# Kernel optimization log

Measured on AMD Instinct MI355X. Metric: run time of the kernel, lower is better.

## Reference

```python
import math
import jax, jax.numpy as jnp
import numpy as np

B, T, D, S = 4, 8192, 1024, 32  # batch, seq, dim, num_slots; segment L = T // S


def setup_inputs() -> dict:
    key = jax.random.key(0)
    ks = jax.random.split(key, 11)
    d_inv_sqrt = D ** -0.5
    return {
        "x": jax.random.normal(ks[0], (B, T, D), jnp.float32),
        "gate_w": jax.random.normal(ks[1], (D, D), jnp.float32) * d_inv_sqrt,
        "gate_b": jnp.zeros((D,), jnp.float32),
        "read_q_w": jax.random.normal(ks[2], (D, D), jnp.float32) * 0.02,
        "read_k_w": jax.random.normal(ks[3], (D, D), jnp.float32) * 0.02,
        "read_v_w": jax.random.normal(ks[4], (D, D), jnp.float32) * 0.02,
        "output_w": jax.random.normal(ks[5], (D, D), jnp.float32) * d_inv_sqrt,
        "memory_slots": jax.random.normal(ks[6], (S, D), jnp.float32) * 0.02,
        "write_q_w": jax.random.normal(ks[7], (D, D), jnp.float32) * 0.02,
        "write_k_w": jax.random.normal(ks[8], (D, D), jnp.float32) * 0.02,
        "write_v_w": jax.random.normal(ks[9], (D, D), jnp.float32) * 0.02,
    }


def reference(x, gate_w, gate_b, read_q_w, read_k_w, read_v_w, output_w,
              memory_slots, write_q_w, write_k_w, write_v_w):
    b, t, d = x.shape
    s = memory_slots.shape[0]
    L = t // s  # segment length
    scale = 1.0 / math.sqrt(d)

    h = x @ gate_w.T + gate_b  # [B,T,D] gate pre-activation

    # --- write: per-slot attention over that slot's segment (block-diagonal) ---
    q = memory_slots @ write_q_w.T                      # [S,D]
    xs = x.reshape(b, s, L, d)                          # [B,S,L,D]
    k = xs @ write_k_w.T                                # [B,S,L,D]
    v = xs @ write_v_w.T                                # [B,S,L,D]
    wqk = jnp.einsum('sd,bsld->bsl', q, k) * scale      # [B,S,L]
    wattn = jax.nn.softmax(wqk, axis=-1)
    memory = jnp.einsum('bsl,bsld->bsd', wattn, v)      # [B,S,D]

    # --- read: masked cross-attention from tokens to memory slots ---
    rq = x @ read_q_w.T                                 # [B,T,D]
    rk = memory @ read_k_w.T                            # [B,S,D]
    rv = memory @ read_v_w.T                            # [B,S,D]
    rqk = jnp.einsum('btd,bsd->bts', rq, rk) * scale    # [B,T,S]
    seg = jnp.arange(t) // L                            # token -> segment index
    mask = seg[:, None] <= jnp.arange(s)[None, :]       # [T,S]; attend to slots >= own segment
    rqk = jnp.where(mask[None, :, :], rqk, -jnp.inf)
    rattn = jax.nn.softmax(rqk, axis=-1)
    read = jnp.einsum('bts,bsd->btd', rattn, rv)        # [B,T,D]

    y = x + jax.nn.sigmoid(h) * read
    out = y @ output_w.T
    return out, memory
```

## Files before the change

kernel.cpp:

```cpp
#include <hip/hip_runtime.h>
#include <stdint.h>

#define TB 4
#define TT 8192
#define TD 1024
#define TS 32
#define TL 256
#define BT 32768

typedef unsigned short u16;
typedef __bf16 bf16x8 __attribute__((ext_vector_type(8)));
typedef float f32x4 __attribute__((ext_vector_type(4)));

typedef uint32_t u32_g __attribute__((address_space(1)));
typedef uint32_t u32_l __attribute__((address_space(3)));

#define VMWAIT(N) asm volatile("s_waitcnt vmcnt(" #N ")" ::: "memory")
#define LGKM0()   asm volatile("s_waitcnt lgkmcnt(0)" ::: "memory")

__device__ __forceinline__ u16 f2b(float f){
  union { float f; uint32_t u; } a; a.f = f;
  uint32_t r = a.u + 0x7FFFu + ((a.u >> 16) & 1u);
  return (u16)(r >> 16);
}
__device__ __forceinline__ float b2f(u16 u){
  union { uint32_t u; float f; } a; a.u = ((uint32_t)u) << 16;
  return a.f;
}
__device__ __forceinline__ void gll16(const void* g, void* l){
  __builtin_amdgcn_global_load_lds((const u32_g*)g, (u32_l*)l, 16, 0, 0);
}

__global__ void k_tran(const float* __restrict__ w0, const float* __restrict__ w1,
                       const float* __restrict__ w2, const float* __restrict__ w3,
                       const float* __restrict__ w4, const float* __restrict__ ms,
                       u16* __restrict__ t0, u16* __restrict__ t1,
                       u16* __restrict__ t2, u16* __restrict__ t3,
                       u16* __restrict__ t4, u16* __restrict__ msb){
  int tid = threadIdx.x, z = blockIdx.z;
  if (z == 5){
    int i = (blockIdx.y*16 + blockIdx.x)*256 + tid;
    if (i < 8192){
      float4 v = ((const float4*)ms)[i];
      ushort4 u; u.x=f2b(v.x); u.y=f2b(v.y); u.z=f2b(v.z); u.w=f2b(v.w);
      ((ushort4*)msb)[i] = u;
    }
    return;
  }
  const float* src = (z==0)?w0:(z==1)?w1:(z==2)?w2:(z==3)?w3:w4;
  u16* dst = (z==0)?t0:(z==1)?t1:(z==2)?t2:(z==3)?t3:t4;
  __shared__ float sT[64][65];
  int r0 = blockIdx.y*64, c0 = blockIdx.x*64;
  int lr = tid >> 2, lc = (tid & 3)*16;
  #pragma unroll
  for (int j=0; j<4; ++j){
    float4 v = *(const float4*)(src + (size_t)(r0+lr)*TD + c0 + lc + j*4);
    sT[lr][lc+j*4+0]=v.x; sT[lr][lc+j*4+1]=v.y; sT[lr][lc+j*4+2]=v.z; sT[lr][lc+j*4+3]=v.w;
  }
  __syncthreads();
  int oc = tid >> 2, orh = (tid & 3)*16;
  #pragma unroll
  for (int j=0; j<4; ++j){
    ushort4 u;
    u.x = f2b(sT[orh+j*4+0][oc]);
    u.y = f2b(sT[orh+j*4+1][oc]);
    u.z = f2b(sT[orh+j*4+2][oc]);
    u.w = f2b(sT[orh+j*4+3][oc]);
    *(ushort4*)(dst + (size_t)(c0+oc)*TD + r0 + orh + j*4) = u;
  }
}

__global__ __launch_bounds__(512) void k_smmw(
    const u16* __restrict__ A0, const u16* __restrict__ W0, u16* __restrict__ O0, int tr0, float s0,
    const u16* __restrict__ A1, const u16* __restrict__ W1, u16* __restrict__ O1, int tr1, float s1){
  const u16 *A, *W; u16* O; int tr; float sc;
  if (blockIdx.z == 0){ A=A0; W=W0; O=O0; tr=tr0; sc=s0; }
  else                { A=A1; W=W1; O=O1; tr=tr1; sc=s1; }
  int tid = threadIdx.x, lane = tid & 63, wv = tid >> 6;
  int r15 = lane & 15, kg = lane >> 4;
  int wr = wv >> 2, wc = wv & 3;
  int m0 = blockIdx.y*128 + wr*64;
  int n0 = blockIdx.x*128 + wc*32;
  const u16* ap = A + (size_t)(m0 + r15)*TD + kg*8;
  const u16* bp = W + (size_t)(n0 + r15)*TD + kg*8;
  f32x4 acc[4][2];
  #pragma unroll
  for (int i=0;i<4;i++){ f32x4 z={0,0,0,0}; acc[i][0]=z; acc[i][1]=z; }
  #pragma unroll 2
  for (int k0=0; k0<TD; k0+=32){
    bf16x8 b0 = *(const bf16x8*)(bp + k0);
    bf16x8 b1 = *(const bf16x8*)(bp + 16*TD + k0);
    bf16x8 a0 = *(const bf16x8*)(ap + k0);
    bf16x8 a1 = *(const bf16x8*)(ap + 16*TD + k0);
    bf16x8 a2 = *(const bf16x8*)(ap + 32*TD + k0);
    bf16x8 a3 = *(const bf16x8*)(ap + 48*TD + k0);
    acc[0][0] = __builtin_amdgcn_mfma_f32_16x16x32_bf16(a0, b0, acc[0][0], 0,0,0);
    acc[0][1] = __builtin_amdgcn_mfma_f32_16x16x32_bf16(a0, b1, acc[0][1], 0,0,0);
    acc[1][0] = __builtin_amdgcn_mfma_f32_16x16x32_bf16(a1, b0, acc[1][0], 0,0,0);
    acc[1][1] = __builtin_amdgcn_mfma_f32_16x16x32_bf16(a1, b1, acc[1][1], 0,0,0);
    acc[2][0] = __builtin_amdgcn_mfma_f32_16x16x32_bf16(a2, b0, acc[2][0], 0,0,0);
    acc[2][1] = __builtin_amdgcn_mfma_f32_16x16x32_bf16(a2, b1, acc[2][1], 0,0,0);
    acc[3][0] = __builtin_amdgcn_mfma_f32_16x16x32_bf16(a3, b0, acc[3][0], 0,0,0);
    acc[3][1] = __builtin_amdgcn_mfma_f32_16x16x32_bf16(a3, b1, acc[3][1], 0,0,0);
  }
  #pragma unroll
  for (int mf=0; mf<4; ++mf){
    #pragma unroll
    for (int nf=0; nf<2; ++nf){
      int n = n0 + nf*16 + r15;
      #pragma unroll
      for (int qq=0; qq<4; ++qq){
        float v = acc[mf][nf][qq]*sc;
        int m = m0 + mf*16 + kg*4 + qq;
        if (tr) O[(size_t)n*TD + m] = f2b(v);
        else    O[(size_t)m*TD + n] = f2b(v);
      }
    }
  }
}

__global__ __launch_bounds__(512) void k_qk32(const u16* __restrict__ msb, const u16* __restrict__ WzT,
                                              float* __restrict__ qkp){
  int tid = threadIdx.x, lane = tid & 63, wv = tid >> 6;
  int r15 = lane & 15, kg = lane >> 4;
  int n0 = blockIdx.x*128 + wv*16;
  int kbase = blockIdx.y*512;
  const u16* ap = msb + (size_t)r15*TD + kbase + kg*8;
  const u16* bp = WzT + (size_t)(n0 + r15)*TD + kbase + kg*8;
  f32x4 a0 = {0,0,0,0}, a1 = {0,0,0,0};
  #pragma unroll 4
  for (int k0=0; k0<512; k0+=32){
    bf16x8 b  = *(const bf16x8*)(bp + k0);
    bf16x8 x0 = *(const bf16x8*)(ap + k0);
    bf16x8 x1 = *(const bf16x8*)(ap + 16*TD + k0);
    a0 = __builtin_amdgcn_mfma_f32_16x16x32_bf16(x0, b, a0, 0,0,0);
    a1 = __builtin_amdgcn_mfma_f32_16x16x32_bf16(x1, b, a1, 0,0,0);
  }
  const float sc = 1.0f/32.0f;
  float* o = qkp + (size_t)blockIdx.y*32768;
  #pragma unroll
  for (int qq=0; qq<4; ++qq){
    o[(size_t)(kg*4 + qq)*TD + n0 + r15]      = a0[qq]*sc;
    o[(size_t)(16 + kg*4 + qq)*TD + n0 + r15] = a1[qq]*sc;
  }
}

__global__ void k_convdot(const float* __restrict__ x, const float* __restrict__ qkp,
                          u16* __restrict__ xb, float* __restrict__ wqk,
                          const float* __restrict__ s0, const float* __restrict__ s1,
                          const float* __restrict__ s2, const float* __restrict__ s3,
                          const float* __restrict__ s4,
                          u16* __restrict__ d0, u16* __restrict__ d1,
                          u16* __restrict__ d2, u16* __restrict__ d3,
                          u16* __restrict__ d4){
  int tid = threadIdx.x;
  if (blockIdx.x >= 2048){
    int i = (blockIdx.x - 2048)*256 + tid;
    int mi = i >> 18, j = i & 262143;
    const float* src; u16* dst;
    if      (mi == 0){ src = s0; dst = d0; }
    else if (mi == 1){ src = s1; dst = d1; }
    else if (mi == 2){ src = s2; dst = d2; }
    else if (mi == 3){ src = s3; dst = d3; }
    else             { src = s4; dst = d4; }
    float4 v = ((const float4*)src)[j];
    ushort4 u; u.x=f2b(v.x); u.y=f2b(v.y); u.z=f2b(v.z); u.w=f2b(v.w);
    ((ushort4*)dst)[j] = u;
    return;
  }
  int lane = tid & 63, wv = tid >> 6;
  long bt0 = (long)blockIdx.x * 16;
  int sseg = (int)((bt0 & (TT-1)) >> 8);
  float qv[16];
  #pragma unroll
  for (int i=0;i<4;i++){
    const float* qp = qkp + (size_t)sseg*TD + i*256 + lane*4;
    float4 ta = *(const float4*)qp;
    float4 tb = *(const float4*)(qp + 32768);
    qv[i*4+0]=ta.x+tb.x; qv[i*4+1]=ta.y+tb.y; qv[i*4+2]=ta.z+tb.z; qv[i*4+3]=ta.w+tb.w;
  }
  for (int tok = wv; tok < 16; tok += 4){
    long bt = bt0 + tok;
    const float* xr = x + bt*TD;
    float dot = 0.f;
    #pragma unroll
    for (int i=0;i<4;i++){
      float4 t = *(const float4*)(xr + i*256 + lane*4);
      ushort4 u; u.x=f2b(t.x); u.y=f2b(t.y); u.z=f2b(t.z); u.w=f2b(t.w);
      *(ushort4*)(xb + bt*TD + i*256 + lane*4) = u;
      dot += t.x*qv[i*4] + t.y*qv[i*4+1] + t.z*qv[i*4+2] + t.w*qv[i*4+3];
    }
    #pragma unroll
    for (int o=32;o;o>>=1) dot += __shfl_xor(dot, o);
    if (lane == 0) wqk[bt] = dot;
  }
}

__global__ __launch_bounds__(512) void k_wattn_smm(
    const float* __restrict__ wqk, const u16* __restrict__ xb, u16* __restrict__ xbarb,
    const u16* __restrict__ A1, const u16* __restrict__ W1, u16* __restrict__ O1,
    const u16* __restrict__ A2, const u16* __restrict__ W2, u16* __restrict__ O2){
  __shared__ float sw[2][TL];
  __shared__ float red[2][8];
  __shared__ f32x4 part[2][4][64];
  int tid = threadIdx.x;
  if (blockIdx.x < 256){
    int u = tid >> 8;
    int unit = blockIdx.x*2 + u;
    int bs = unit >> 2, dch = unit & 3;
    int b = bs >> 5, s = bs & 31;
    int t2 = tid & 255, lane = t2 & 63, wv = t2 >> 6;
    long base = (long)b*TT + (long)s*TL;
    float v = wqk[base + t2];
    float m = v;
    #pragma unroll
    for (int o=32;o;o>>=1) m = fmaxf(m, __shfl_xor(m, o));
    if (lane == 0) red[u][wv] = m;
    __syncthreads();
    m = fmaxf(fmaxf(red[u][0], red[u][1]), fmaxf(red[u][2], red[u][3]));
    float e = __expf(v - m);
    float sm = e;
    #pragma unroll
    for (int o=32;o;o>>=1) sm += __shfl_xor(sm, o);
    if (lane == 0) red[u][4+wv] = sm;
    __syncthreads();
    sm = red[u][4]+red[u][5]+red[u][6]+red[u][7];
    sw[u][t2] = e / sm;
    __syncthreads();
    int d = dch*256 + lane*4;
    const u16* xp = xb + (base + wv*64)*TD + d;
    f32x4 acc = {0,0,0,0};
    #pragma unroll 8
    for (int i=0; i<64; ++i){
      float w = sw[u][wv*64 + i];
      ushort4 uu = *(const ushort4*)(xp + (size_t)i*TD);
      acc[0] += w*b2f(uu.x); acc[1] += w*b2f(uu.y); acc[2] += w*b2f(uu.z); acc[3] += w*b2f(uu.w);
    }
    part[u][wv][lane] = acc;
    __syncthreads();
    if (wv == 0){
      f32x4 t0 = part[u][0][lane], t1 = part[u][1][lane], t2v = part[u][2][lane], t3 = part[u][3][lane];
      ushort4 o;
      o.x = f2b(t0[0]+t1[0]+t2v[0]+t3[0]);
      o.y = f2b(t0[1]+t1[1]+t2v[1]+t3[1]);
      o.z = f2b(t0[2]+t1[2]+t2v[2]+t3[2]);
      o.w = f2b(t0[3]+t1[3]+t2v[3]+t3[3]);
      *(ushort4*)(xbarb + ((size_t)b*TS + s)*TD + d) = o;
    }
    return;
  }
  int bi = blockIdx.x - 256;
  const u16 *A, *W; u16* O; int tr;
  if (bi < 64){ A=A1; W=W1; O=O1; tr=0; }
  else        { A=A2; W=W2; O=O2; tr=1; bi -= 64; }
  int by = bi >> 3, bx = bi & 7;
  int lane = tid & 63, wv = tid >> 6;
  int r15 = lane & 15, kg = lane >> 4;
  int wr = wv >> 2, wc = wv & 3;
  int m0 = by*128 + wr*64;
  int n0 = bx*128 + wc*32;
  const u16* ap = A + (size_t)(m0 + r15)*TD + kg*8;
  const u16* bp = W + (size_t)(n0 + r15)*TD + kg*8;
  f32x4 acc[4][2];
  #pragma unroll
  for (int i=0;i<4;i++){ f32x4 z={0,0,0,0}; acc[i][0]=z; acc[i][1]=z; }
  #pragma unroll 2
  for (int k0=0; k0<TD; k0+=32){
    bf16x8 b0 = *(const bf16x8*)(bp + k0);
    bf16x8 b1 = *(const bf16x8*)(bp + 16*TD + k0);
    bf16x8 a0 = *(const bf16x8*)(ap + k0);
    bf16x8 a1 = *(const bf16x8*)(ap + 16*TD + k0);
    bf16x8 a2 = *(const bf16x8*)(ap + 32*TD + k0);
    bf16x8 a3 = *(const bf16x8*)(ap + 48*TD + k0);
    acc[0][0] = __builtin_amdgcn_mfma_f32_16x16x32_bf16(a0, b0, acc[0][0], 0,0,0);
    acc[0][1] = __builtin_amdgcn_mfma_f32_16x16x32_bf16(a0, b1, acc[0][1], 0,0,0);
    acc[1][0] = __builtin_amdgcn_mfma_f32_16x16x32_bf16(a1, b0, acc[1][0], 0,0,0);
    acc[1][1] = __builtin_amdgcn_mfma_f32_16x16x32_bf16(a1, b1, acc[1][1], 0,0,0);
    acc[2][0] = __builtin_amdgcn_mfma_f32_16x16x32_bf16(a2, b0, acc[2][0], 0,0,0);
    acc[2][1] = __builtin_amdgcn_mfma_f32_16x16x32_bf16(a2, b1, acc[2][1], 0,0,0);
    acc[3][0] = __builtin_amdgcn_mfma_f32_16x16x32_bf16(a3, b0, acc[3][0], 0,0,0);
    acc[3][1] = __builtin_amdgcn_mfma_f32_16x16x32_bf16(a3, b1, acc[3][1], 0,0,0);
  }
  #pragma unroll
  for (int mf=0; mf<4; ++mf){
    #pragma unroll
    for (int nf=0; nf<2; ++nf){
      int n = n0 + nf*16 + r15;
      #pragma unroll
      for (int qq=0; qq<4; ++qq){
        float v = acc[mf][nf][qq];
        int m = m0 + mf*16 + kg*4 + qq;
        if (tr) O[(size_t)n*TD + m] = f2b(v);
        else    O[(size_t)m*TD + n] = f2b(v);
      }
    }
  }
}

__global__ __launch_bounds__(512) void k_xbar3(const u16* __restrict__ xbarb,
                                               const u16* __restrict__ Wv, const u16* __restrict__ WdT,
                                               const u16* __restrict__ We,
                                               float* __restrict__ memo, u16* __restrict__ rkb,
                                               u16* __restrict__ rvT){
  int z = blockIdx.z;
  const u16* W = (z==0) ? Wv : (z==1) ? WdT : We;
  int tid = threadIdx.x, lane = tid & 63, wv = tid >> 6;
  int r15 = lane & 15, kg = lane >> 4;
  int wr = wv >> 2, wc = wv & 3;
  int n0 = blockIdx.x*128 + wc*32;
  const u16* ap = xbarb + (size_t)(wr*64 + r15)*TD + kg*8;
  const u16* bp = W + (size_t)(n0 + r15)*TD + kg*8;
  f32x4 acc[4][2];
  #pragma unroll
  for (int i=0;i<4;i++){ f32x4 zz={0,0,0,0}; acc[i][0]=zz; acc[i][1]=zz; }
  #pragma unroll 2
  for (int k0=0; k0<TD; k0+=32){
    bf16x8 b0 = *(const bf16x8*)(bp + k0);
    bf16x8 b1 = *(const bf16x8*)(bp + 16*TD + k0);
    bf16x8 a0 = *(const bf16x8*)(ap + k0);
    bf16x8 a1 = *(const bf16x8*)(ap + 16*TD + k0);
    bf16x8 a2 = *(const bf16x8*)(ap + 32*TD + k0);
    bf16x8 a3 = *(const bf16x8*)(ap + 48*TD + k0);
    acc[0][0] = __builtin_amdgcn_mfma_f32_16x16x32_bf16(a0, b0, acc[0][0], 0,0,0);
    acc[0][1] = __builtin_amdgcn_mfma_f32_16x16x32_bf16(a0, b1, acc[0][1], 0,0,0);
    acc[1][0] = __builtin_amdgcn_mfma_f32_16x16x32_bf16(a1, b0, acc[1][0], 0,0,0);
    acc[1][1] = __builtin_amdgcn_mfma_f32_16x16x32_bf16(a1, b1, acc[1][1], 0,0,0);
    acc[2][0] = __builtin_amdgcn_mfma_f32_16x16x32_bf16(a2, b0, acc[2][0], 0,0,0);
    acc[2][1] = __builtin_amdgcn_mfma_f32_16x16x32_bf16(a2, b1, acc[2][1], 0,0,0);
    acc[3][0] = __builtin_amdgcn_mfma_f32_16x16x32_bf16(a3, b0, acc[3][0], 0,0,0);
    acc[3][1] = __builtin_amdgcn_mfma_f32_16x16x32_bf16(a3, b1, acc[3][1], 0,0,0);
  }
  #pragma unroll
  for (int mf=0; mf<4; ++mf){
    #pragma unroll
    for (int nf=0; nf<2; ++nf){
      int n = n0 + nf*16 + r15;
      #pragma unroll
      for (int qq=0; qq<4; ++qq){
        float v = acc[mf][nf][qq];
        int m = wr*64 + mf*16 + kg*4 + qq;
        if (z == 0)      memo[(size_t)m*TD + n] = v;
        else if (z == 1) rkb[(size_t)m*TD + n] = f2b(v);
        else             rvT[((size_t)(m>>5)*TD + n)*TS + (m&31)] = f2b(v);
      }
    }
  }
}

template<bool SIG>
__global__ __launch_bounds__(512, 2) void k_gemm(const u16* __restrict__ A, const u16* __restrict__ Bw,
                                                 const float* __restrict__ bias, void* __restrict__ Cp,
                                                 const u16* __restrict__ rkb, const u16* __restrict__ rvT){
  __shared__ __align__(16) char sL[131072];
  int tid = threadIdx.x, lane = tid & 63, wv = tid >> 6;
  int bid = blockIdx.x;
  int wg = ((bid & 7) << 6) | (bid >> 3);
  int nt = wg & 3, mt = wg >> 2;
  int m0 = mt*256, n0 = nt*256;
  int wr = wv >> 2, wc = wv & 3;
  int r15 = lane & 15, kg = lane >> 4;
  int smin = (m0 & (TT-1)) >> 8;
  bool wcP = SIG && ((wr == 0) ? (wc < 2) : (wc >= 2));

  int ard[8], brd[4];
  #pragma unroll
  for (int i=0;i<8;i++){ int row = wr*128 + i*16 + r15; ard[i] = row*128 + ((kg ^ (row&7))<<4); }
  #pragma unroll
  for (int j=0;j<4;j++){ int row = wc*64  + j*16 + r15; brd[j] = row*128 + ((kg ^ (row&7))<<4); }

  const u16* asrc[4]; const u16* bsrc[4]; int ldst[4];
  #pragma unroll
  for (int r=0;r<4;r++){
    int Sp  = r*512 + tid;
    int row = Sp >> 3;
    int kq  = (Sp & 7) ^ (row & 7);
    asrc[r] = A  + (size_t)(m0 + row)*TD + kq*8;
    bsrc[r] = Bw + (size_t)(n0 + row)*TD + kq*8;
    ldst[r] = Sp*16;
  }
  const u16* rkp = rkb + (size_t)((m0 >> 13)*TS + (wc&1)*16 + r15)*TD + kg*8;

  f32x4 acc[8][4];
  #pragma unroll
  for (int i=0;i<8;i++){
    #pragma unroll
    for (int j=0;j<4;j++){ f32x4 z = {0,0,0,0}; acc[i][j] = z; }
  }
  f32x4 pacc[8];
  if constexpr (SIG){
    #pragma unroll
    for (int i=0;i<8;i++){ f32x4 z = {0,0,0,0}; pacc[i] = z; }
  }

  auto stage = [&](int t){
    char* slot = sL + (size_t)(t&1)*65536;
    int k0 = t*64;
    #pragma unroll
    for (int r=0;r<4;r++) gll16(asrc[r] + k0, slot + ldst[r]);
    #pragma unroll
    for (int r=0;r<4;r++) gll16(bsrc[r] + k0, slot + 32768 + ldst[r]);
  };

  auto compute = [&](int t, bf16x8 rk0, bf16x8 rk1){
    const char* sa = sL + (size_t)(t&1)*65536;
    const char* sb = sa + 32768;
    bf16x8 bfg[4], af[4];
    #pragma unroll
    for (int j=0;j<4;j++) bfg[j] = *(const bf16x8*)(sb + brd[j]);
    #pragma unroll
    for (int i=0;i<4;i++) af[i] = *(const bf16x8*)(sa + ard[i]);
    LGKM0();
    __builtin_amdgcn_sched_barrier(0);
    __builtin_amdgcn_s_setprio(1);
    #pragma unroll
    for (int i=0;i<4;i++){
      #pragma unroll
      for (int j=0;j<4;j++)
        acc[i][j] = __builtin_amdgcn_mfma_f32_16x16x32_bf16(af[i], bfg[j], acc[i][j], 0,0,0);
    }
    if constexpr (SIG){
      if (wcP){
        #pragma unroll
        for (int i=0;i<4;i++) pacc[i] = __builtin_amdgcn_mfma_f32_16x16x32_bf16(af[i], rk0, pacc[i], 0,0,0);
      }
    }
    __builtin_amdgcn_s_setprio(0);
    bf16x8 af2[4];
    #pragma unroll
    for (int i=0;i<4;i++) af2[i] = *(const bf16x8*)(sa + (ard[4+i]));
    LGKM0();
    __builtin_amdgcn_sched_barrier(0);
    __builtin_amdgcn_s_setprio(1);
    #pragma unroll
    for (int i=0;i<4;i++){
      #pragma unroll
      for (int j=0;j<4;j++)
        acc[4+i][j] = __builtin_amdgcn_mfma_f32_16x16x32_bf16(af2[i], bfg[j], acc[4+i][j], 0,0,0);
    }
    if constexpr (SIG){
      if (wcP){
        #pragma unroll
        for (int i=0;i<4;i++) pacc[4+i] = __builtin_amdgcn_mfma_f32_16x16x32_bf16(af2[i], rk0, pacc[4+i], 0,0,0);
      }
    }
    __builtin_amdgcn_s_setprio(0);
    bf16x8 bfh[4], ag[4];
    #pragma unroll
    for (int j=0;j<4;j++) bfh[j] = *(const bf16x8*)(sb + (brd[j]^64));
    #pragma unroll
    for (int i=0;i<4;i++) ag[i] = *(const bf16x8*)(sa + (ard[i]^64));
    LGKM0();
    __builtin_amdgcn_sched_barrier(0);
    __builtin_amdgcn_s_setprio(1);
    #pragma unroll
    for (int i=0;i<4;i++){
      #pragma unroll
      for (int j=0;j<4;j++)
        acc[i][j] = __builtin_amdgcn_mfma_f32_16x16x32_bf16(ag[i], bfh[j], acc[i][j], 0,0,0);
    }
    if constexpr (SIG){
      if (wcP){
        #pragma unroll
        for (int i=0;i<4;i++) pacc[i] = __builtin_amdgcn_mfma_f32_16x16x32_bf16(ag[i], rk1, pacc[i], 0,0,0);
      }
    }
    __builtin_amdgcn_s_setprio(0);
    bf16x8 ag2[4];
    #pragma unroll
    for (int i=0;i<4;i++) ag2[i] = *(const bf16x8*)(sa + (ard[4+i]^64));
    LGKM0();
    __builtin_amdgcn_sched_barrier(0);
    __builtin_amdgcn_s_setprio(1);
    #pragma unroll
    for (int i=0;i<4;i++){
      #pragma unroll
      for (int j=0;j<4;j++)
        acc[4+i][j] = __builtin_amdgcn_mfma_f32_16x16x32_bf16(ag2[i], bfh[j], acc[4+i][j], 0,0,0);
    }
    if constexpr (SIG){
      if (wcP){
        #pragma unroll
        for (int i=0;i<4;i++) pacc[4+i] = __builtin_amdgcn_mfma_f32_16x16x32_bf16(ag2[i], rk1, pacc[4+i], 0,0,0);
      }
    }
    __builtin_amdgcn_s_setprio(0);
  };

  stage(0);
  for (int t=0; t<16; ++t){
    if (t > 0) __builtin_amdgcn_s_barrier();
    bf16x8 rk0, rk1;
    if (wcP){
      rk0 = *(const bf16x8*)(rkp + t*64);
      rk1 = *(const bf16x8*)(rkp + t*64 + 32);
      __builtin_amdgcn_sched_barrier(0);
    }
    if (t < 15){
      stage(t+1);
      VMWAIT(8);
    } else {
      VMWAIT(0);
    }
    __builtin_amdgcn_sched_barrier(0);
    __builtin_amdgcn_s_barrier();
    compute(t, rk0, rk1);
  }

  if constexpr (SIG){
    float* Pf = (float*)sL;
    u16* Pb16 = (u16*)(sL + 33792);
    __syncthreads();
    if (wcP){
      #pragma unroll
      for (int i=0;i<8;i++){
        int tok = wr*128 + i*16 + kg*4;
        #pragma unroll
        for (int q=0;q<4;q++)
          Pf[(tok+q)*33 + (wc&1)*16 + r15] = pacc[i][q];
      }
    }
    __syncthreads();
    if (tid < 256){
      float v[32];
      float mx = -1e30f;
      #pragma unroll
      for (int s=0;s<32;s++){
        float t = Pf[tid*33 + s];
        v[s] = t;
        if (s >= smin) mx = fmaxf(mx, t);
      }
      float sum = 0.f;
      #pragma unroll
      for (int s=0;s<32;s++){
        float e = (s >= smin) ? __expf(v[s]-mx) : 0.f;
        v[s] = e; sum += e;
      }
      float rs = 1.f/sum;
      #pragma unroll
      for (int s=0;s<32;s++) Pb16[tid*40 + s] = f2b(v[s]*rs);
    }
    __syncthreads();

    int b = m0 >> 13;
    bf16x8 vfrag[4];
    #pragma unroll
    for (int j=0;j<4;j++){
      int n = n0 + wc*64 + j*16 + r15;
      vfrag[j] = *(const bf16x8*)(rvT + ((size_t)b*TD + n)*TS + kg*8);
    }
    #pragma unroll
    for (int i=0;i<8;i++){
      bf16x8 pfrag = *(const bf16x8*)(Pb16 + (wr*128 + i*16 + r15)*40 + kg*8);
      f32x4 rd[4];
      #pragma unroll
      for (int j=0;j<4;j++){
        f32x4 z = {0,0,0,0};
        rd[j] = __builtin_amdgcn_mfma_f32_16x16x32_bf16(pfrag, vfrag[j], z, 0,0,0);
      }
      int mrow = m0 + wr*128 + i*16 + kg*4;
      #pragma unroll
      for (int j=0;j<4;j++){
        int n = n0 + wc*64 + j*16 + r15;
        float bj = bias[n];
        #pragma unroll
        for (int q=0;q<4;q++){
          float g = 1.f/(1.f + __expf(-(acc[i][j][q] + bj)));
          size_t idx = (size_t)(mrow + q)*TD + n;
          float xv = b2f(A[idx]);
          ((u16*)Cp)[idx] = f2b(xv + g*rd[j][q]);
        }
      }
    }
  } else {
    #pragma unroll
    for (int i=0;i<8;i++){
      int mrow = m0 + wr*128 + i*16 + kg*4;
      #pragma unroll
      for (int j=0;j<4;j++){
        int n = n0 + wc*64 + j*16 + r15;
        #pragma unroll
        for (int q=0;q<4;q++){
          size_t idx = (size_t)(mrow + q)*TD + n;
          ((float*)Cp)[idx] = acc[i][j][q];
        }
      }
    }
  }
}

extern "C" void kernel_launch(void* const* d_in, const int* in_sizes, int n_in,
                              void* d_out, int out_size, void* d_ws, size_t ws_size,
                              hipStream_t stream){
  const float* x   = (const float*)d_in[0];
  const float* gw  = (const float*)d_in[1];
  const float* gb  = (const float*)d_in[2];
  const float* rqw = (const float*)d_in[3];
  const float* rkw = (const float*)d_in[4];
  const float* rvw = (const float*)d_in[5];
  const float* ow  = (const float*)d_in[6];
  const float* ms  = (const float*)d_in[7];
  const float* wqw = (const float*)d_in[8];
  const float* wkw = (const float*)d_in[9];
  const float* wvw = (const float*)d_in[10];
  float* out = (float*)d_out;
  float* mem_out = out + (size_t)BT*TD;

  char* o = (char*)d_out;
  u16* xb    = (u16*)o;
  u16* gwb   = (u16*)(o + 69206016);
  u16* wvwb  = (u16*)(o + 71303168);
  u16* rkwb  = (u16*)(o + 73400320);
  u16* rvwb  = (u16*)(o + 75497472);
  u16* xbarb = (u16*)(o + 79757312);
  u16* rvT   = (u16*)(o + 80281600);
  u16* WvT   = (u16*)(o + 84934656);
  u16* WrqT  = (u16*)(o + 87031808);
  u16* WqT   = (u16*)(o + 89128960);
  u16* WkT   = (u16*)(o + 91226112);
  u16* We    = (u16*)(o + 95420416);
  u16* WdT   = (u16*)(o + 97517568);
  u16* WzT   = (u16*)(o + 99614720);
  u16* msb   = (u16*)(o + 101711872);
  u16* WrkT  = (u16*)(o + 103809024);
  u16* WgT   = (u16*)(o + 105906176);

  char* w = (char*)d_ws;
  u16*   gy    = (u16*)(w);
  float* wqkb  = (float*)(w + 67108864);
  float* qkp   = (float*)(w + 67239936);
  u16*   rkb   = (u16*)(w + 67502080);
  u16*   owb   = (u16*)(w + 68288512);

  k_tran<<<dim3(16,16,6),256,0,stream>>>(wvw, rqw, wqw, wkw, rkw, ms,
                                         WvT, WrqT, WqT, WkT, WrkT, msb);
  k_smmw<<<dim3(8,8,2),512,0,stream>>>(WqT, WkT, WzT, 1, 1.f,
                                       WrkT, WrqT, WgT, 1, 1.f/32.f);
  k_qk32<<<dim3(8,2),512,0,stream>>>(msb, WzT, qkp);
  k_convdot<<<7168,256,0,stream>>>(x, qkp, xb, wqkb,
                                   gw, ow, wvw, rkw, rvw,
                                   gwb, owb, wvwb, rkwb, rvwb);
  k_wattn_smm<<<384,512,0,stream>>>(wqkb, xb, xbarb,
                                    rvwb, WvT, We,
                                    WvT, WgT, WdT);
  k_xbar3<<<dim3(8,1,3),512,0,stream>>>(xbarb, wvwb, WdT, We, mem_out, rkb, rvT);
  k_gemm<true><<<512,512,0,stream>>>(xb, gwb, gb, gy, rkb, rvT);
  k_gemm<false><<<512,512,0,stream>>>(gy, owb, nullptr, d_out, nullptr, nullptr);
}
```

Measured before the change: 388.8 us.

## Split read-attention softmax into separate kernel and widen GEMM blocks to 1024 threads

Moves the token-to-memory-slot score computation and masked softmax out of the gated GEMM into a new standalone kernel, k_pattn, which writes bf16 probabilities to a spare output region. The gated GEMM then only loads these probabilities in its epilogue, which removes the extra per-wave MFMAs, the warp imbalance and the LDS softmax phase. Both GEMMs now use 1024-thread blocks, with each wave owning a 64x64 sub-tile instead of 128x64. This lowers per-wave register pressure and adds more waves per block. In exchange there is an extra kernel launch, a second pass over the bf16 activations to compute scores, and a round trip of the probabilities through global memory.

```diff
diff --git a/kernel.cpp b/kernel.cpp
--- a/kernel.cpp
+++ b/kernel.cpp
@@ -347,10 +347,51 @@
   }
 }
 
+__global__ __launch_bounds__(256) void k_pattn(const u16* __restrict__ xb, const u16* __restrict__ rkb,
+                                               u16* __restrict__ P){
+  int tid = threadIdx.x, lane = tid & 63, wv = tid >> 6;
+  long bt0 = (long)blockIdx.x * 64;
+  int b = (int)(bt0 >> 13);
+  int smin = (int)((bt0 & (TT-1)) >> 8);
+  int r15 = lane & 15, kg = lane >> 4;
+
+  long tw = bt0 + wv*16;
+  const u16* ap  = xb  + (size_t)(tw + r15)*TD + kg*8;
+  const u16* bp0 = rkb + ((size_t)(b*TS + r15))*TD + kg*8;
+  const u16* bp1 = rkb + ((size_t)(b*TS + 16 + r15))*TD + kg*8;
+  f32x4 p0 = {0,0,0,0}, p1 = {0,0,0,0};
+  #pragma unroll 4
+  for (int ks=0; ks<32; ++ks){
+    bf16x8 a  = *(const bf16x8*)(ap  + ks*32);
+    bf16x8 b0 = *(const bf16x8*)(bp0 + ks*32);
+    bf16x8 b1 = *(const bf16x8*)(bp1 + ks*32);
+    p0 = __builtin_amdgcn_mfma_f32_16x16x32_bf16(a, b0, p0, 0,0,0);
+    p1 = __builtin_amdgcn_mfma_f32_16x16x32_bf16(a, b1, p1, 0,0,0);
+  }
+  bool msk0 = (r15 < smin), msk1 = (16 + r15 < smin);
+  #pragma unroll
+  for (int q=0;q<4;q++){
+    float l0 = msk0 ? -1e30f : p0[q];
+    float l1 = msk1 ? -1e30f : p1[q];
+    float mx = fmaxf(l0, l1);
+    #pragma unroll
+    for (int o=1;o<16;o<<=1) mx = fmaxf(mx, __shfl_xor(mx, o));
+    float e0 = msk0 ? 0.f : __expf(l0 - mx);
+    float e1 = msk1 ? 0.f : __expf(l1 - mx);
+    float smv = e0 + e1;
+    #pragma unroll
+    for (int o=1;o<16;o<<=1) smv += __shfl_xor(smv, o);
+    float rs = 1.f/smv;
+    long trow = tw + 4*kg + q;
+    P[trow*TS + r15]      = f2b(e0*rs);
+    P[trow*TS + 16 + r15] = f2b(e1*rs);
+  }
+}
+
 template<bool SIG>
-__global__ __launch_bounds__(512, 2) void k_gemm(const u16* __restrict__ A, const u16* __restrict__ Bw,
-                                                 const float* __restrict__ bias, void* __restrict__ Cp,
-                                                 const u16* __restrict__ rkb, const u16* __restrict__ rvT){
+__global__ __launch_bounds__(1024) void k_gemm(const u16* __restrict__ A, const u16* __restrict__ Bw,
+                                               const float* __restrict__ bias, void* __restrict__ Cp,
+                                               const u16* __restrict__ P, const u16* __restrict__ rvT){
   __shared__ __align__(16) char sL[131072];
   int tid = threadIdx.x, lane = tid & 63, wv = tid >> 6;
   int bid = blockIdx.x;
@@ -359,49 +400,41 @@
   int m0 = mt*256, n0 = nt*256;
   int wr = wv >> 2, wc = wv & 3;
   int r15 = lane & 15, kg = lane >> 4;
-  int smin = (m0 & (TT-1)) >> 8;
-  bool wcP = SIG && ((wr == 0) ? (wc < 2) : (wc >= 2));
-
-  int ard[8], brd[4];
-  #pragma unroll
-  for (int i=0;i<8;i++){ int row = wr*128 + i*16 + r15; ard[i] = row*128 + ((kg ^ (row&7))<<4); }
-  #pragma unroll
-  for (int j=0;j<4;j++){ int row = wc*64  + j*16 + r15; brd[j] = row*128 + ((kg ^ (row&7))<<4); }
-
-  const u16* asrc[4]; const u16* bsrc[4]; int ldst[4];
-  #pragma unroll
-  for (int r=0;r<4;r++){
-    int Sp  = r*512 + tid;
+
+  int ard[4], brd[4];
+  #pragma unroll
+  for (int i=0;i<4;i++){ int row = wr*64 + i*16 + r15; ard[i] = row*128 + ((kg ^ (row&7))<<4); }
+  #pragma unroll
+  for (int j=0;j<4;j++){ int row = wc*64 + j*16 + r15; brd[j] = row*128 + ((kg ^ (row&7))<<4); }
+
+  const u16* asrc[2]; const u16* bsrc[2]; int ldst[2];
+  #pragma unroll
+  for (int r=0;r<2;r++){
+    int Sp  = r*1024 + tid;
     int row = Sp >> 3;
     int kq  = (Sp & 7) ^ (row & 7);
     asrc[r] = A  + (size_t)(m0 + row)*TD + kq*8;
     bsrc[r] = Bw + (size_t)(n0 + row)*TD + kq*8;
     ldst[r] = Sp*16;
   }
-  const u16* rkp = rkb + (size_t)((m0 >> 13)*TS + (wc&1)*16 + r15)*TD + kg*8;
-
-  f32x4 acc[8][4];
-  #pragma unroll
-  for (int i=0;i<8;i++){
+
+  f32x4 acc[4][4];
+  #pragma unroll
+  for (int i=0;i<4;i++){
     #pragma unroll
     for (int j=0;j<4;j++){ f32x4 z = {0,0,0,0}; acc[i][j] = z; }
-  }
-  f32x4 pacc[8];
-  if constexpr (SIG){
-    #pragma unroll
-    for (int i=0;i<8;i++){ f32x4 z = {0,0,0,0}; pacc[i] = z; }
   }
 
   auto stage = [&](int t){
     char* slot = sL + (size_t)(t&1)*65536;
     int k0 = t*64;
-    #pragma unroll
-    for (int r=0;r<4;r++) gll16(asrc[r] + k0, slot + ldst[r]);
-    #pragma unroll
-    for (int r=0;r<4;r++) gll16(bsrc[r] + k0, slot + 32768 + ldst[r]);
+    gll16(asrc[0] + k0, slot + ldst[0]);
+    gll16(asrc[1] + k0, slot + ldst[1]);
+    gll16(bsrc[0] + k0, slot + 32768 + ldst[0]);
+    gll16(bsrc[1] + k0, slot + 32768 + ldst[1]);
   };
 
-  auto compute = [&](int t, bf16x8 rk0, bf16x8 rk1){
+  auto compute = [&](int t){
     const char* sa = sL + (size_t)(t&1)*65536;
     const char* sb = sa + 32768;
     bf16x8 bfg[4], af[4];
@@ -418,31 +451,6 @@
       for (int j=0;j<4;j++)
         acc[i][j] = __builtin_amdgcn_mfma_f32_16x16x32_bf16(af[i], bfg[j], acc[i][j], 0,0,0);
     }
-    if constexpr (SIG){
-      if (wcP){
-        #pragma unroll
-        for (int i=0;i<4;i++) pacc[i] = __builtin_amdgcn_mfma_f32_16x16x32_bf16(af[i], rk0, pacc[i], 0,0,0);
-      }
-    }
-    __builtin_amdgcn_s_setprio(0);
-    bf16x8 af2[4];
-    #pragma unroll
-    for (int i=0;i<4;i++) af2[i] = *(const bf16x8*)(sa + (ard[4+i]));
-    LGKM0();
-    __builtin_amdgcn_sched_barrier(0);
-    __builtin_amdgcn_s_setprio(1);
-    #pragma unroll
-    for (int i=0;i<4;i++){
-      #pragma unroll
-      for (int j=0;j<4;j++)
-        acc[4+i][j] = __builtin_amdgcn_mfma_f32_16x16x32_bf16(af2[i], bfg[j], acc[4+i][j], 0,0,0);
-    }
-    if constexpr (SIG){
-      if (wcP){
-        #pragma unroll
-        for (int i=0;i<4;i++) pacc[4+i] = __builtin_amdgcn_mfma_f32_16x16x32_bf16(af2[i], rk0, pacc[4+i], 0,0,0);
-      }
-    }
     __builtin_amdgcn_s_setprio(0);
     bf16x8 bfh[4], ag[4];
     #pragma unroll
@@ -458,89 +466,23 @@
       for (int j=0;j<4;j++)
         acc[i][j] = __builtin_amdgcn_mfma_f32_16x16x32_bf16(ag[i], bfh[j], acc[i][j], 0,0,0);
     }
-    if constexpr (SIG){
-      if (wcP){
-        #pragma unroll
-        for (int i=0;i<4;i++) pacc[i] = __builtin_amdgcn_mfma_f32_16x16x32_bf16(ag[i], rk1, pacc[i], 0,0,0);
-      }
-    }
-    __builtin_amdgcn_s_setprio(0);
-    bf16x8 ag2[4];
-    #pragma unroll
-    for (int i=0;i<4;i++) ag2[i] = *(const bf16x8*)(sa + (ard[4+i]^64));
-    LGKM0();
-    __builtin_amdgcn_sched_barrier(0);
-    __builtin_amdgcn_s_setprio(1);
-    #pragma unroll
-    for (int i=0;i<4;i++){
-      #pragma unroll
-      for (int j=0;j<4;j++)
-        acc[4+i][j] = __builtin_amdgcn_mfma_f32_16x16x32_bf16(ag2[i], bfh[j], acc[4+i][j], 0,0,0);
-    }
-    if constexpr (SIG){
-      if (wcP){
-        #pragma unroll
-        for (int i=0;i<4;i++) pacc[4+i] = __builtin_amdgcn_mfma_f32_16x16x32_bf16(ag2[i], rk1, pacc[4+i], 0,0,0);
-      }
-    }
     __builtin_amdgcn_s_setprio(0);
   };
 
   stage(0);
   for (int t=0; t<16; ++t){
     if (t > 0) __builtin_amdgcn_s_barrier();
-    bf16x8 rk0, rk1;
-    if (wcP){
-      rk0 = *(const bf16x8*)(rkp + t*64);
-      rk1 = *(const bf16x8*)(rkp + t*64 + 32);
-      __builtin_amdgcn_sched_barrier(0);
-    }
     if (t < 15){
       stage(t+1);
-      VMWAIT(8);
+      VMWAIT(4);
     } else {
       VMWAIT(0);
     }
-    __builtin_amdgcn_sched_barrier(0);
     __builtin_amdgcn_s_barrier();
-    compute(t, rk0, rk1);
-  }
-
-  if constexpr (SIG){
-    float* Pf = (float*)sL;
-    u16* Pb16 = (u16*)(sL + 33792);
-    __syncthreads();
-    if (wcP){
-      #pragma unroll
-      for (int i=0;i<8;i++){
-        int tok = wr*128 + i*16 + kg*4;
-        #pragma unroll
-        for (int q=0;q<4;q++)
-          Pf[(tok+q)*33 + (wc&1)*16 + r15] = pacc[i][q];
-      }
-    }
-    __syncthreads();
-    if (tid < 256){
-      float v[32];
-      float mx = -1e30f;
-      #pragma unroll
-      for (int s=0;s<32;s++){
-        float t = Pf[tid*33 + s];
-        v[s] = t;
-        if (s >= smin) mx = fmaxf(mx, t);
-      }
-      float sum = 0.f;
-      #pragma unroll
-      for (int s=0;s<32;s++){
-        float e = (s >= smin) ? __expf(v[s]-mx) : 0.f;
-        v[s] = e; sum += e;
-      }
-      float rs = 1.f/sum;
-      #pragma unroll
-      for (int s=0;s<32;s++) Pb16[tid*40 + s] = f2b(v[s]*rs);
-    }
-    __syncthreads();
-
+    compute(t);
+  }
+
+  if (SIG){
     int b = m0 >> 13;
     bf16x8 vfrag[4];
     #pragma unroll
@@ -549,15 +491,16 @@
       vfrag[j] = *(const bf16x8*)(rvT + ((size_t)b*TD + n)*TS + kg*8);
     }
     #pragma unroll
-    for (int i=0;i<8;i++){
-      bf16x8 pfrag = *(const bf16x8*)(Pb16 + (wr*128 + i*16 + r15)*40 + kg*8);
+    for (int i=0;i<4;i++){
+      int tokbase = m0 + wr*64 + i*16;
+      bf16x8 pfrag = *(const bf16x8*)(P + (size_t)(tokbase + r15)*TS + kg*8);
       f32x4 rd[4];
       #pragma unroll
       for (int j=0;j<4;j++){
         f32x4 z = {0,0,0,0};
         rd[j] = __builtin_amdgcn_mfma_f32_16x16x32_bf16(pfrag, vfrag[j], z, 0,0,0);
       }
-      int mrow = m0 + wr*128 + i*16 + kg*4;
+      int mrow = tokbase + kg*4;
       #pragma unroll
       for (int j=0;j<4;j++){
         int n = n0 + wc*64 + j*16 + r15;
@@ -573,8 +516,8 @@
     }
   } else {
     #pragma unroll
-    for (int i=0;i<8;i++){
-      int mrow = m0 + wr*128 + i*16 + kg*4;
+    for (int i=0;i<4;i++){
+      int mrow = m0 + wr*64 + i*16 + kg*4;
       #pragma unroll
       for (int j=0;j<4;j++){
         int n = n0 + wc*64 + j*16 + r15;
@@ -607,6 +550,7 @@
 
   char* o = (char*)d_out;
   u16* xb    = (u16*)o;
+  u16* Pb    = (u16*)(o + 67108864);
   u16* gwb   = (u16*)(o + 69206016);
   u16* wvwb  = (u16*)(o + 71303168);
   u16* rkwb  = (u16*)(o + 73400320);
@@ -643,6 +587,7 @@
                                     rvwb, WvT, We,
                                     WvT, WgT, WdT);
   k_xbar3<<<dim3(8,1,3),512,0,stream>>>(xbarb, wvwb, WdT, We, mem_out, rkb, rvT);
-  k_gemm<true><<<512,512,0,stream>>>(xb, gwb, gb, gy, rkb, rvT);
-  k_gemm<false><<<512,512,0,stream>>>(gy, owb, nullptr, d_out, nullptr, nullptr);
-}
+  k_pattn<<<512,256,0,stream>>>(xb, rkb, Pb);
+  k_gemm<true><<<512,1024,0,stream>>>(xb, gwb, gb, gy, Pb, rvT);
+  k_gemm<false><<<512,1024,0,stream>>>(gy, owb, nullptr, d_out, nullptr, nullptr);
+}
```

Measured after the change: 416.9 us. 1.07x slower.
